# Optimization experiments

Measured on AMD Instinct MI355X. Metric: run time of the kernel, lower is better.

## Reference

```python
import jax, jax.numpy as jnp
import numpy as np

N = 8192
F_IN = 256
F_OUT = 128
SLOPE = 0.2
NEG_INF = -9000000000000000.0


def setup_inputs() -> dict:
    key = jax.random.key(0)
    k1, k2, k3, k4, k5 = jax.random.split(key, 5)
    x = jax.random.normal(k1, (N, F_IN), dtype=jnp.float32)
    adj = jax.random.randint(k2, (N, N), 0, 2).astype(jnp.float32)
    W = jax.random.normal(k3, (F_IN, F_OUT), dtype=jnp.float32) * (1.0 / np.sqrt(F_IN))
    a_src = jax.random.normal(k4, (F_OUT,), dtype=jnp.float32) * (1.0 / np.sqrt(F_OUT))
    a_dst = jax.random.normal(k5, (F_OUT,), dtype=jnp.float32) * (1.0 / np.sqrt(F_OUT))
    return {"x": x, "adj": adj, "W": W, "a_src": a_src, "a_dst": a_dst}


def reference(x, adj, W, a_src, a_dst):
    # h: (N, F_OUT)
    h = x @ W
    f_src = h @ a_src  # (N,)
    f_dst = h @ a_dst  # (N,)
    # additive attention scores: (N, N)
    e = f_src[:, None] + f_dst[None, :]
    e = jnp.where(e >= 0, e, SLOPE * e)  # leaky_relu
    e = jnp.where(adj > 0, e, NEG_INF)
    alpha = jax.nn.softmax(e, axis=1)  # (N, N)
    return alpha @ h  # (N, F_OUT)
```

## Files before the change

### kernel.cpp

```cpp
#include <hip/hip_runtime.h>
#include <hip/hip_bf16.h>

#define NN 8192
#define FIN 256
#define FO 128
#define KSPLIT 8
#define JCHUNK (NN / KSPLIT)
#define L2E 1.4426950408889634f
#define C2  0.28853900817779268f

typedef __bf16 bf16x8 __attribute__((ext_vector_type(8)));
typedef __bf16 bf16x2 __attribute__((ext_vector_type(2)));
typedef float  f32x4  __attribute__((ext_vector_type(4)));

__global__ __launch_bounds__(256) void k_proj(
    const float* __restrict__ x, const float* __restrict__ W,
    const float* __restrict__ a_src, const float* __restrict__ a_dst,
    __bf16* __restrict__ Bp, float* __restrict__ f_src, float* __restrict__ f_dst)
{
  __shared__ float xs[16 * FIN];
  __shared__ float fs[16], fd[16];
  const int tid = threadIdx.x;
  const int i0 = blockIdx.x * 16;

  const float4* xg = (const float4*)(x + (size_t)i0 * FIN);
  float4* xs4 = (float4*)xs;
  #pragma unroll
  for (int t = 0; t < 4; t++) xs4[tid + 256 * t] = xg[tid + 256 * t];
  if (tid < 16) { fs[tid] = 0.f; fd[tid] = 0.f; }
  __syncthreads();

  const int cq = tid & 31;
  const int rg = tid >> 5;
  const int c0 = cq * 4;
  const int r0 = rg * 2;
  float acc0[4] = {0.f,0.f,0.f,0.f};
  float acc1[4] = {0.f,0.f,0.f,0.f};
  const float* xr0 = xs + r0 * FIN;
  const float* xr1 = xs + (r0 + 1) * FIN;

  for (int k = 0; k < FIN; k += 4) {
    float4 xa = *(const float4*)(xr0 + k);
    float4 xb = *(const float4*)(xr1 + k);
    #pragma unroll
    for (int kk = 0; kk < 4; kk++) {
      float4 wv = *(const float4*)(W + (size_t)(k + kk) * FO + c0);
      float xav = ((const float*)&xa)[kk];
      float xbv = ((const float*)&xb)[kk];
      acc0[0] += xav * wv.x; acc0[1] += xav * wv.y;
      acc0[2] += xav * wv.z; acc0[3] += xav * wv.w;
      acc1[0] += xbv * wv.x; acc1[1] += xbv * wv.y;
      acc1[2] += xbv * wv.z; acc1[3] += xbv * wv.w;
    }
  }

  float4 as = *(const float4*)(a_src + c0);
  float4 ad = *(const float4*)(a_dst + c0);
  float ps0 = acc0[0]*as.x + acc0[1]*as.y + acc0[2]*as.z + acc0[3]*as.w;
  float ps1 = acc1[0]*as.x + acc1[1]*as.y + acc1[2]*as.z + acc1[3]*as.w;
  float pd0 = acc0[0]*ad.x + acc0[1]*ad.y + acc0[2]*ad.z + acc0[3]*ad.w;
  float pd1 = acc1[0]*ad.x + acc1[1]*ad.y + acc1[2]*ad.z + acc1[3]*ad.w;
  atomicAdd(&fs[r0],     ps0);
  atomicAdd(&fs[r0 + 1], ps1);
  atomicAdd(&fd[r0],     pd0);
  atomicAdd(&fd[r0 + 1], pd1);

  const int j0 = i0 + r0;
  const int kg = j0 >> 5;
  const int q  = (j0 >> 3) & 3;
  const int t0 = j0 & 7;
  #pragma unroll
  for (int c = 0; c < 4; c++) {
    const int n = c0 + c;
    bf16x2 v;
    v[0] = (__bf16)acc0[c];
    v[1] = (__bf16)acc1[c];
    size_t idx = ((size_t)(kg * 8 + (n >> 4)) * 64 + q * 16 + (n & 15)) * 8 + t0;
    *(bf16x2*)(Bp + idx) = v;
  }
  __syncthreads();
  if (tid < 16) { f_src[i0 + tid] = fs[tid]; f_dst[i0 + tid] = fd[tid]; }
}

__global__ __launch_bounds__(256, 4) void k_attn(
    const float* __restrict__ adj, const __bf16* __restrict__ Bp,
    const float* __restrict__ f_src, const float* __restrict__ f_dst,
    float* __restrict__ num, float* __restrict__ lsum)
{
  __shared__ float G1[JCHUNK];
  __shared__ float G2[JCHUNK];
  const int tid = threadIdx.x;
  const int rb = blockIdx.x >> 3;
  const int ks = blockIdx.x & 7;
  const int jbase = ks * JCHUNK;

  #pragma unroll
  for (int t = 0; t < 4; t++) {
    int j = tid + t * 256;
    float d = f_dst[jbase + j];
    G1[j] = __builtin_amdgcn_exp2f(d * L2E);
    G2[j] = __builtin_amdgcn_exp2f(d * C2);
  }

  const int w = tid >> 6;
  const int lane = tid & 63;
  const int m = lane & 15;
  const int q = lane >> 4;
  const int i0 = rb * 64 + w * 16;
  const float s  = f_src[i0 + m];
  const float F1 = __builtin_amdgcn_exp2f(s * L2E);
  const float F2 = __builtin_amdgcn_exp2f(s * C2);

  f32x4 acc[8];
  #pragma unroll
  for (int t = 0; t < 8; t++) acc[t] = (f32x4){0.f, 0.f, 0.f, 0.f};
  float psum = 0.f;

  const float* adjp = adj + (size_t)(i0 + m) * NN + jbase + q * 8;
  const float* g1p = G1 + q * 8;
  const float* g2p = G2 + q * 8;
  const __bf16* bb = Bp + (size_t)(jbase >> 5) * 4096 + lane * 8;

  __syncthreads();

  float4 cur0 = *(const float4*)(adjp + 0);
  float4 cur1 = *(const float4*)(adjp + 4);
  float4 cur2 = *(const float4*)(adjp + 32);
  float4 cur3 = *(const float4*)(adjp + 36);

  #pragma unroll 2
  for (int st = 0; st < 16; ++st) {
    float4 nxt0, nxt1, nxt2, nxt3;
    if (st < 15) {
      const float* ap = adjp + (st + 1) * 64;
      nxt0 = *(const float4*)(ap + 0);
      nxt1 = *(const float4*)(ap + 4);
      nxt2 = *(const float4*)(ap + 32);
      nxt3 = *(const float4*)(ap + 36);
    }
    #pragma unroll
    for (int g = 0; g < 2; ++g) {
      const int ko = st * 64 + g * 32;
      float4 a0 = g ? cur2 : cur0;
      float4 a1 = g ? cur3 : cur1;
      float4 u0 = *(const float4*)(g1p + ko);
      float4 u1 = *(const float4*)(g1p + ko + 4);
      float4 v0 = *(const float4*)(g2p + ko);
      float4 v1 = *(const float4*)(g2p + ko + 4);
      float p0 = (a0.x > 0.f) ? fmaxf(F1 * u0.x, F2 * v0.x) : 0.f;
      float p1 = (a0.y > 0.f) ? fmaxf(F1 * u0.y, F2 * v0.y) : 0.f;
      float p2 = (a0.z > 0.f) ? fmaxf(F1 * u0.z, F2 * v0.z) : 0.f;
      float p3 = (a0.w > 0.f) ? fmaxf(F1 * u0.w, F2 * v0.w) : 0.f;
      float p4 = (a1.x > 0.f) ? fmaxf(F1 * u1.x, F2 * v1.x) : 0.f;
      float p5 = (a1.y > 0.f) ? fmaxf(F1 * u1.y, F2 * v1.y) : 0.f;
      float p6 = (a1.z > 0.f) ? fmaxf(F1 * u1.z, F2 * v1.z) : 0.f;
      float p7 = (a1.w > 0.f) ? fmaxf(F1 * u1.w, F2 * v1.w) : 0.f;
      psum += ((p0 + p1) + (p2 + p3)) + ((p4 + p5) + (p6 + p7));

      bf16x8 af;
      af[0] = (__bf16)p0; af[1] = (__bf16)p1; af[2] = (__bf16)p2; af[3] = (__bf16)p3;
      af[4] = (__bf16)p4; af[5] = (__bf16)p5; af[6] = (__bf16)p6; af[7] = (__bf16)p7;

      const __bf16* bs = bb + (size_t)(st * 2 + g) * 4096;
      #pragma unroll
      for (int nt = 0; nt < 8; nt++) {
        bf16x8 bfrag = *(const bf16x8*)(bs + nt * 512);
        acc[nt] = __builtin_amdgcn_mfma_f32_16x16x32_bf16(af, bfrag, acc[nt], 0, 0, 0);
      }
    }
    if (st < 15) { cur0 = nxt0; cur1 = nxt1; cur2 = nxt2; cur3 = nxt3; }
  }

  psum += __shfl_xor(psum, 16);
  psum += __shfl_xor(psum, 32);
  if (lane < 16) atomicAdd(&lsum[i0 + lane], psum);

  #pragma unroll
  for (int nt = 0; nt < 8; nt++) {
    #pragma unroll
    for (int r = 0; r < 4; r++) {
      atomicAdd(&num[(size_t)(i0 + q * 4 + r) * FO + nt * 16 + m], acc[nt][r]);
    }
  }
}

__global__ __launch_bounds__(256) void k_div(
    const float* __restrict__ num, const float* __restrict__ lsum,
    float* __restrict__ out)
{
  int idx = blockIdx.x * 256 + threadIdx.x;
  float4 v = ((const float4*)num)[idx];
  float inv = 1.0f / lsum[idx >> 5];
  float4 o;
  o.x = v.x * inv; o.y = v.y * inv; o.z = v.z * inv; o.w = v.w * inv;
  ((float4*)out)[idx] = o;
}

extern "C" void kernel_launch(void* const* d_in, const int* in_sizes, int n_in,
                              void* d_out, int out_size, void* d_ws, size_t ws_size,
                              hipStream_t stream) {
  const float* x     = (const float*)d_in[0];
  const float* adj   = (const float*)d_in[1];
  const float* W     = (const float*)d_in[2];
  const float* a_src = (const float*)d_in[3];
  const float* a_dst = (const float*)d_in[4];
  float* out = (float*)d_out;

  char* ws = (char*)d_ws;
  __bf16* Bp   = (__bf16*)ws;
  float* f_src = (float*)(ws + 2097152);
  float* f_dst = (float*)(ws + 2097152 + 32768);
  float* num   = (float*)(ws + 2097152 + 65536);
  float* lsum  = (float*)(ws + 2097152 + 65536 + 4194304);

  hipMemsetAsync(num, 0, 4194304 + 32768, stream);
  hipLaunchKernelGGL(k_proj, dim3(512), dim3(256), 0, stream,
                     x, W, a_src, a_dst, Bp, f_src, f_dst);
  hipLaunchKernelGGL(k_attn, dim3(1024), dim3(256), 0, stream,
                     adj, Bp, f_src, f_dst, num, lsum);
  hipLaunchKernelGGL(k_div, dim3(1024), dim3(256), 0, stream,
                     num, lsum, out);
}
```

Baseline: 451.3 us.

## Process 32 rows per wave and stage adj tiles into LDS via DMA

Each wave now covers two 16-row M-tiles, so every B fragment loaded from global memory feeds two MFMAs instead of one. This halves B traffic per unit of output. The adjacency tile is double-buffered into per-wave LDS using global_load_lds, which should overlap the adj stream with compute. The grid shrinks to 512 blocks with launch bounds of 2, raising register use and lowering the number of resident waves available to hide latency. The barrier may also force waits on the prefetch that was just issued, which would cut into the intended overlap.

```diff
diff --git a/kernel.cpp b/kernel.cpp
--- a/kernel.cpp
+++ b/kernel.cpp
@@ -5,13 +5,21 @@
 #define FIN 256
 #define FO 128
 #define KSPLIT 8
-#define JCHUNK (NN / KSPLIT)
+#define JCHUNK 1024
+#define NSTEP 16
+#define GSTRIDE 260
 #define L2E 1.4426950408889634f
 #define C2  0.28853900817779268f
 
 typedef __bf16 bf16x8 __attribute__((ext_vector_type(8)));
 typedef __bf16 bf16x2 __attribute__((ext_vector_type(2)));
 typedef float  f32x4  __attribute__((ext_vector_type(4)));
+
+__device__ __forceinline__ void dma16(const float* g, float* l) {
+  __builtin_amdgcn_global_load_lds(
+      (__attribute__((address_space(1))) void*)g,
+      (__attribute__((address_space(3))) void*)l, 16, 0, 0);
+}
 
 __global__ __launch_bounds__(256) void k_proj(
     const float* __restrict__ x, const float* __restrict__ W,
@@ -82,16 +90,19 @@
   if (tid < 16) { f_src[i0 + tid] = fs[tid]; f_dst[i0 + tid] = fd[tid]; }
 }
 
-__global__ __launch_bounds__(256, 4) void k_attn(
+__global__ __launch_bounds__(256, 2) void k_attn(
     const float* __restrict__ adj, const __bf16* __restrict__ Bp,
     const float* __restrict__ f_src, const float* __restrict__ f_dst,
     float* __restrict__ num, float* __restrict__ lsum)
 {
   __shared__ float G1[JCHUNK];
   __shared__ float G2[JCHUNK];
+  __shared__ __align__(16) float atile[4][2][8 * GSTRIDE];
+
   const int tid = threadIdx.x;
   const int rb = blockIdx.x >> 3;
   const int ks = blockIdx.x & 7;
+  const int i0 = rb * 128;
   const int jbase = ks * JCHUNK;
 
   #pragma unroll
@@ -106,80 +117,103 @@
   const int lane = tid & 63;
   const int m = lane & 15;
   const int q = lane >> 4;
-  const int i0 = rb * 64 + w * 16;
-  const float s  = f_src[i0 + m];
-  const float F1 = __builtin_amdgcn_exp2f(s * L2E);
-  const float F2 = __builtin_amdgcn_exp2f(s * C2);
-
-  f32x4 acc[8];
-  #pragma unroll
-  for (int t = 0; t < 8; t++) acc[t] = (f32x4){0.f, 0.f, 0.f, 0.f};
-  float psum = 0.f;
-
-  const float* adjp = adj + (size_t)(i0 + m) * NN + jbase + q * 8;
-  const float* g1p = G1 + q * 8;
-  const float* g2p = G2 + q * 8;
-  const __bf16* bb = Bp + (size_t)(jbase >> 5) * 4096 + lane * 8;
-
-  __syncthreads();
-
-  float4 cur0 = *(const float4*)(adjp + 0);
-  float4 cur1 = *(const float4*)(adjp + 4);
-  float4 cur2 = *(const float4*)(adjp + 32);
-  float4 cur3 = *(const float4*)(adjp + 36);
-
-  #pragma unroll 2
-  for (int st = 0; st < 16; ++st) {
-    float4 nxt0, nxt1, nxt2, nxt3;
-    if (st < 15) {
-      const float* ap = adjp + (st + 1) * 64;
-      nxt0 = *(const float4*)(ap + 0);
-      nxt1 = *(const float4*)(ap + 4);
-      nxt2 = *(const float4*)(ap + 32);
-      nxt3 = *(const float4*)(ap + 36);
-    }
-    #pragma unroll
-    for (int g = 0; g < 2; ++g) {
-      const int ko = st * 64 + g * 32;
-      float4 a0 = g ? cur2 : cur0;
-      float4 a1 = g ? cur3 : cur1;
-      float4 u0 = *(const float4*)(g1p + ko);
-      float4 u1 = *(const float4*)(g1p + ko + 4);
-      float4 v0 = *(const float4*)(g2p + ko);
-      float4 v1 = *(const float4*)(g2p + ko + 4);
-      float p0 = (a0.x > 0.f) ? fmaxf(F1 * u0.x, F2 * v0.x) : 0.f;
-      float p1 = (a0.y > 0.f) ? fmaxf(F1 * u0.y, F2 * v0.y) : 0.f;
-      float p2 = (a0.z > 0.f) ? fmaxf(F1 * u0.z, F2 * v0.z) : 0.f;
-      float p3 = (a0.w > 0.f) ? fmaxf(F1 * u0.w, F2 * v0.w) : 0.f;
-      float p4 = (a1.x > 0.f) ? fmaxf(F1 * u1.x, F2 * v1.x) : 0.f;
-      float p5 = (a1.y > 0.f) ? fmaxf(F1 * u1.y, F2 * v1.y) : 0.f;
-      float p6 = (a1.z > 0.f) ? fmaxf(F1 * u1.z, F2 * v1.z) : 0.f;
-      float p7 = (a1.w > 0.f) ? fmaxf(F1 * u1.w, F2 * v1.w) : 0.f;
-      psum += ((p0 + p1) + (p2 + p3)) + ((p4 + p5) + (p6 + p7));
-
-      bf16x8 af;
-      af[0] = (__bf16)p0; af[1] = (__bf16)p1; af[2] = (__bf16)p2; af[3] = (__bf16)p3;
-      af[4] = (__bf16)p4; af[5] = (__bf16)p5; af[6] = (__bf16)p6; af[7] = (__bf16)p7;
-
-      const __bf16* bs = bb + (size_t)(st * 2 + g) * 4096;
+  const int wbase = i0 + w * 32;
+
+  float F1[2], F2[2];
+  #pragma unroll
+  for (int mt = 0; mt < 2; mt++) {
+    float s = f_src[wbase + mt * 16 + m];
+    F1[mt] = __builtin_amdgcn_exp2f(s * L2E);
+    F2[mt] = __builtin_amdgcn_exp2f(s * C2);
+  }
+
+  f32x4 acc[2][8];
+  #pragma unroll
+  for (int mt = 0; mt < 2; mt++)
+    #pragma unroll
+    for (int nt = 0; nt < 8; nt++) acc[mt][nt] = (f32x4){0.f, 0.f, 0.f, 0.f};
+  float psum[2] = {0.f, 0.f};
+
+  const float* gsrc = adj + (size_t)(wbase + (lane >> 4)) * NN + jbase + (lane & 15) * 4;
+  float* tw0 = &atile[w][0][0];
+  float* tw1 = &atile[w][1][0];
+
+#define ISSUE(buf, step)                                                      \
+  {                                                                           \
+    const float* gs = gsrc + (step) * 64;                                     \
+    float* lb = (buf) ? tw1 : tw0;                                            \
+    _Pragma("unroll")                                                         \
+    for (int g = 0; g < 8; g++)                                               \
+      dma16(gs + (size_t)g * 4 * NN, lb + g * GSTRIDE);                       \
+  }
+
+  ISSUE(0, 0)
+
+  for (int step = 0; step < NSTEP; ++step) {
+    const int buf = step & 1;
+    if (step + 1 < NSTEP) ISSUE(buf ^ 1, step + 1)
+    __syncthreads();
+
+    const float* tb = buf ? tw1 : tw0;
+    #pragma unroll
+    for (int kg = 0; kg < 2; kg++) {
+      const int jj = step * 64 + kg * 32 + q * 8;
+      float4 u0 = *(const float4*)(G1 + jj);
+      float4 u1 = *(const float4*)(G1 + jj + 4);
+      float4 v0 = *(const float4*)(G2 + jj);
+      float4 v1 = *(const float4*)(G2 + jj + 4);
+
+      bf16x8 af[2];
+      #pragma unroll
+      for (int mt = 0; mt < 2; mt++) {
+        const int r = mt * 16 + m;
+        const float* ap = tb + (r >> 2) * GSTRIDE + (r & 3) * 64 + kg * 32 + q * 8;
+        float4 a0 = *(const float4*)ap;
+        float4 a1 = *(const float4*)(ap + 4);
+        const float f1 = F1[mt], f2 = F2[mt];
+        float p0 = (a0.x > 0.f) ? fmaxf(f1 * u0.x, f2 * v0.x) : 0.f;
+        float p1 = (a0.y > 0.f) ? fmaxf(f1 * u0.y, f2 * v0.y) : 0.f;
+        float p2 = (a0.z > 0.f) ? fmaxf(f1 * u0.z, f2 * v0.z) : 0.f;
+        float p3 = (a0.w > 0.f) ? fmaxf(f1 * u0.w, f2 * v0.w) : 0.f;
+        float p4 = (a1.x > 0.f) ? fmaxf(f1 * u1.x, f2 * v1.x) : 0.f;
+        float p5 = (a1.y > 0.f) ? fmaxf(f1 * u1.y, f2 * v1.y) : 0.f;
+        float p6 = (a1.z > 0.f) ? fmaxf(f1 * u1.z, f2 * v1.z) : 0.f;
+        float p7 = (a1.w > 0.f) ? fmaxf(f1 * u1.w, f2 * v1.w) : 0.f;
+        psum[mt] += ((p0 + p1) + (p2 + p3)) + ((p4 + p5) + (p6 + p7));
+        bf16x8 a;
+        a[0] = (__bf16)p0; a[1] = (__bf16)p1; a[2] = (__bf16)p2; a[3] = (__bf16)p3;
+        a[4] = (__bf16)p4; a[5] = (__bf16)p5; a[6] = (__bf16)p6; a[7] = (__bf16)p7;
+        af[mt] = a;
+      }
+
+      const __bf16* bsrc = Bp + (size_t)(ks * 32 + step * 2 + kg) * 4096 + lane * 8;
       #pragma unroll
       for (int nt = 0; nt < 8; nt++) {
-        bf16x8 bfrag = *(const bf16x8*)(bs + nt * 512);
-        acc[nt] = __builtin_amdgcn_mfma_f32_16x16x32_bf16(af, bfrag, acc[nt], 0, 0, 0);
+        bf16x8 bfrag = *(const bf16x8*)(bsrc + nt * 512);
+        acc[0][nt] = __builtin_amdgcn_mfma_f32_16x16x32_bf16(af[0], bfrag, acc[0][nt], 0, 0, 0);
+        acc[1][nt] = __builtin_amdgcn_mfma_f32_16x16x32_bf16(af[1], bfrag, acc[1][nt], 0, 0, 0);
       }
     }
-    if (st < 15) { cur0 = nxt0; cur1 = nxt1; cur2 = nxt2; cur3 = nxt3; }
-  }
-
-  psum += __shfl_xor(psum, 16);
-  psum += __shfl_xor(psum, 32);
-  if (lane < 16) atomicAdd(&lsum[i0 + lane], psum);
-
-  #pragma unroll
-  for (int nt = 0; nt < 8; nt++) {
-    #pragma unroll
-    for (int r = 0; r < 4; r++) {
-      atomicAdd(&num[(size_t)(i0 + q * 4 + r) * FO + nt * 16 + m], acc[nt][r]);
+  }
+#undef ISSUE
+
+  #pragma unroll
+  for (int mt = 0; mt < 2; mt++) {
+    float p = psum[mt];
+    p += __shfl_xor(p, 16);
+    p += __shfl_xor(p, 32);
+    if (lane < 16) atomicAdd(&lsum[wbase + mt * 16 + lane], p);
+  }
+
+  #pragma unroll
+  for (int mt = 0; mt < 2; mt++) {
+    const int rb0 = wbase + mt * 16 + q * 4;
+    #pragma unroll
+    for (int nt = 0; nt < 8; nt++) {
+      #pragma unroll
+      for (int r = 0; r < 4; r++) {
+        atomicAdd(&num[(size_t)(rb0 + r) * FO + nt * 16 + m], acc[mt][nt][r]);
+      }
     }
   }
 }
@@ -216,7 +250,7 @@
   hipMemsetAsync(num, 0, 4194304 + 32768, stream);
   hipLaunchKernelGGL(k_proj, dim3(512), dim3(256), 0, stream,
                      x, W, a_src, a_dst, Bp, f_src, f_dst);
-  hipLaunchKernelGGL(k_attn, dim3(1024), dim3(256), 0, stream,
+  hipLaunchKernelGGL(k_attn, dim3(512), dim3(256), 0, stream,
                      adj, Bp, f_src, f_dst, num, lsum);
   hipLaunchKernelGGL(k_div, dim3(1024), dim3(256), 0, stream,
                      num, lsum, out);
```

Result: no change. 448.4 us (-0.6%).

## Split columns across waves in-block and fuse normalization into attention kernel

Applied to the files above, without the earlier changes.

Each attention block now owns 16 rows, and its four waves each cover a quarter of the columns. Partial accumulators are reduced in shared memory and normalized in place, which removes the global atomics, the memset and the separate divide kernel. The exp of f_dst is precomputed once in the projection kernel and read from global memory instead of being rebuilt per block in LDS. The trade-off is a grid of only 512 blocks with a 2-wave-per-SIMD launch bound, each running longer loops, which lowers parallelism and latency hiding for the adjacency stream.

```diff
diff --git a/kernel.cpp b/kernel.cpp
--- a/kernel.cpp
+++ b/kernel.cpp
@@ -4,8 +4,8 @@
 #define NN 8192
 #define FIN 256
 #define FO 128
-#define KSPLIT 8
-#define JCHUNK (NN / KSPLIT)
+#define JCHUNK 2048
+#define NSTEP 32
 #define L2E 1.4426950408889634f
 #define C2  0.28853900817779268f
 
@@ -16,7 +16,8 @@
 __global__ __launch_bounds__(256) void k_proj(
     const float* __restrict__ x, const float* __restrict__ W,
     const float* __restrict__ a_src, const float* __restrict__ a_dst,
-    __bf16* __restrict__ Bp, float* __restrict__ f_src, float* __restrict__ f_dst)
+    __bf16* __restrict__ Bp, float* __restrict__ f_src,
+    float* __restrict__ g1, float* __restrict__ g2)
 {
   __shared__ float xs[16 * FIN];
   __shared__ float fs[16], fd[16];
@@ -79,34 +80,34 @@
     *(bf16x2*)(Bp + idx) = v;
   }
   __syncthreads();
-  if (tid < 16) { f_src[i0 + tid] = fs[tid]; f_dst[i0 + tid] = fd[tid]; }
+  if (tid < 16) {
+    float d = fd[tid];
+    f_src[i0 + tid] = fs[tid];
+    g1[i0 + tid] = __builtin_amdgcn_exp2f(d * L2E);
+    g2[i0 + tid] = __builtin_amdgcn_exp2f(d * C2);
+  }
 }
 
-__global__ __launch_bounds__(256, 4) void k_attn(
+__global__ __launch_bounds__(256, 2) void k_attn(
     const float* __restrict__ adj, const __bf16* __restrict__ Bp,
-    const float* __restrict__ f_src, const float* __restrict__ f_dst,
-    float* __restrict__ num, float* __restrict__ lsum)
+    const float* __restrict__ f_src, const float* __restrict__ g1,
+    const float* __restrict__ g2, float* __restrict__ out)
 {
-  __shared__ float G1[JCHUNK];
-  __shared__ float G2[JCHUNK];
+  __shared__ float accbuf[16 * FO];
+  __shared__ float lred[16];
   const int tid = threadIdx.x;
-  const int rb = blockIdx.x >> 3;
-  const int ks = blockIdx.x & 7;
-  const int jbase = ks * JCHUNK;
-
-  #pragma unroll
-  for (int t = 0; t < 4; t++) {
-    int j = tid + t * 256;
-    float d = f_dst[jbase + j];
-    G1[j] = __builtin_amdgcn_exp2f(d * L2E);
-    G2[j] = __builtin_amdgcn_exp2f(d * C2);
-  }
+  const int i0 = blockIdx.x * 16;
+
+  ((float4*)accbuf)[tid]       = (float4){0.f, 0.f, 0.f, 0.f};
+  ((float4*)accbuf)[tid + 256] = (float4){0.f, 0.f, 0.f, 0.f};
+  if (tid < 16) lred[tid] = 0.f;
 
   const int w = tid >> 6;
   const int lane = tid & 63;
   const int m = lane & 15;
   const int q = lane >> 4;
-  const int i0 = rb * 64 + w * 16;
+  const int jbase = w * JCHUNK;
+
   const float s  = f_src[i0 + m];
   const float F1 = __builtin_amdgcn_exp2f(s * L2E);
   const float F2 = __builtin_amdgcn_exp2f(s * C2);
@@ -117,8 +118,8 @@
   float psum = 0.f;
 
   const float* adjp = adj + (size_t)(i0 + m) * NN + jbase + q * 8;
-  const float* g1p = G1 + q * 8;
-  const float* g2p = G2 + q * 8;
+  const float* g1p = g1 + jbase + q * 8;
+  const float* g2p = g2 + jbase + q * 8;
   const __bf16* bb = Bp + (size_t)(jbase >> 5) * 4096 + lane * 8;
 
   __syncthreads();
@@ -129,9 +130,9 @@
   float4 cur3 = *(const float4*)(adjp + 36);
 
   #pragma unroll 2
-  for (int st = 0; st < 16; ++st) {
+  for (int st = 0; st < NSTEP; ++st) {
     float4 nxt0, nxt1, nxt2, nxt3;
-    if (st < 15) {
+    if (st < NSTEP - 1) {
       const float* ap = adjp + (st + 1) * 64;
       nxt0 = *(const float4*)(ap + 0);
       nxt1 = *(const float4*)(ap + 4);
@@ -168,32 +169,31 @@
         acc[nt] = __builtin_amdgcn_mfma_f32_16x16x32_bf16(af, bfrag, acc[nt], 0, 0, 0);
       }
     }
-    if (st < 15) { cur0 = nxt0; cur1 = nxt1; cur2 = nxt2; cur3 = nxt3; }
+    if (st < NSTEP - 1) { cur0 = nxt0; cur1 = nxt1; cur2 = nxt2; cur3 = nxt3; }
   }
 
   psum += __shfl_xor(psum, 16);
   psum += __shfl_xor(psum, 32);
-  if (lane < 16) atomicAdd(&lsum[i0 + lane], psum);
+  if (lane < 16) atomicAdd(&lred[lane], psum);
 
   #pragma unroll
   for (int nt = 0; nt < 8; nt++) {
     #pragma unroll
     for (int r = 0; r < 4; r++) {
-      atomicAdd(&num[(size_t)(i0 + q * 4 + r) * FO + nt * 16 + m], acc[nt][r]);
-    }
-  }
-}
-
-__global__ __launch_bounds__(256) void k_div(
-    const float* __restrict__ num, const float* __restrict__ lsum,
-    float* __restrict__ out)
-{
-  int idx = blockIdx.x * 256 + threadIdx.x;
-  float4 v = ((const float4*)num)[idx];
-  float inv = 1.0f / lsum[idx >> 5];
-  float4 o;
-  o.x = v.x * inv; o.y = v.y * inv; o.z = v.z * inv; o.w = v.w * inv;
-  ((float4*)out)[idx] = o;
+      atomicAdd(&accbuf[(q * 4 + r) * FO + nt * 16 + m], acc[nt][r]);
+    }
+  }
+  __syncthreads();
+
+  #pragma unroll
+  for (int t = 0; t < 2; t++) {
+    const int idx = tid + t * 256;
+    const float inv = 1.0f / lred[idx >> 5];
+    float4 v = ((const float4*)accbuf)[idx];
+    float4 o;
+    o.x = v.x * inv; o.y = v.y * inv; o.z = v.z * inv; o.w = v.w * inv;
+    ((float4*)(out + (size_t)i0 * FO))[idx] = o;
+  }
 }
 
 extern "C" void kernel_launch(void* const* d_in, const int* in_sizes, int n_in,
@@ -209,15 +209,11 @@
   char* ws = (char*)d_ws;
   __bf16* Bp   = (__bf16*)ws;
   float* f_src = (float*)(ws + 2097152);
-  float* f_dst = (float*)(ws + 2097152 + 32768);
-  float* num   = (float*)(ws + 2097152 + 65536);
-  float* lsum  = (float*)(ws + 2097152 + 65536 + 4194304);
-
-  hipMemsetAsync(num, 0, 4194304 + 32768, stream);
+  float* g1    = (float*)(ws + 2097152 + 32768);
+  float* g2    = (float*)(ws + 2097152 + 65536);
+
   hipLaunchKernelGGL(k_proj, dim3(512), dim3(256), 0, stream,
-                     x, W, a_src, a_dst, Bp, f_src, f_dst);
-  hipLaunchKernelGGL(k_attn, dim3(1024), dim3(256), 0, stream,
-                     adj, Bp, f_src, f_dst, num, lsum);
-  hipLaunchKernelGGL(k_div, dim3(1024), dim3(256), 0, stream,
-                     num, lsum, out);
+                     x, W, a_src, a_dst, Bp, f_src, g1, g2);
+  hipLaunchKernelGGL(k_attn, dim3(512), dim3(256), 0, stream,
+                     adj, Bp, f_src, g1, g2, out);
 }
```

Measured after the change: 469.7 us. +4.1%, slower.
